# Kernel optimization log

Hardware: AMD Instinct MI355X
Metric: run time of the kernel (lower is better)

Reference implementation:

```python
import jax, jax.numpy as jnp
import numpy as np
import math

B, S, D, H = 2, 2048, 1024, 16
DK = D // H


def setup_inputs() -> dict:
    key = jax.random.key(0)
    k1, k2, k3, k4, k5, k6 = jax.random.split(key, 6)
    scale = 1.0 / math.sqrt(D)
    return {
        "query": jax.random.normal(k1, (B, S, D), dtype=jnp.float32),
        "key": jax.random.normal(k2, (B, S, D), dtype=jnp.float32),
        "value": jax.random.normal(k3, (B, S, D), dtype=jnp.float32),
        "Wqkv": jax.random.normal(k4, (D, D), dtype=jnp.float32) * scale,
        "Wout": jax.random.normal(k5, (D, D), dtype=jnp.float32) * scale,
        "mask": jax.random.randint(k6, (B, 1, S, S), 0, 2, dtype=jnp.int32),
    }


def reference(query, key, value, Wqkv, Wout, mask):
    # Single shared QKV projection (same weight applied to q, k, v), no bias.
    q = query @ Wqkv.T
    k = key @ Wqkv.T
    v = value @ Wqkv.T
    # Faithful to the original: reshape (B, S, D) -> (B, H, S, DK) directly
    # (torch .reshape(n_batches, h, -1, d_k), NOT view+transpose).
    q = q.reshape(B, H, S, DK)
    k = k.reshape(B, H, S, DK)
    v = v.reshape(B, H, S, DK)
    scores = jnp.einsum("bhqd,bhkd->bhqk", q, k) / math.sqrt(DK)
    scores = jnp.where(mask == 0, jnp.float32(-1e9), scores)
    p_attn = jax.nn.softmax(scores, axis=-1)  # dropout is identity in eval
    x = jnp.einsum("bhqk,bhkd->bhqd", p_attn, v)  # [B,H,S,DK]
    x = x.transpose(0, 2, 1, 3).reshape(B, S, H * DK)
    return x @ Wout.T
```

## Files before the change

kernel.cpp:

```cpp
#include <hip/hip_runtime.h>
#include <stdint.h>


typedef __bf16 bf16;
typedef __bf16 bf16x8 __attribute__((ext_vector_type(8)));
typedef __bf16 bf16x4 __attribute__((ext_vector_type(4)));
typedef float f32x4 __attribute__((ext_vector_type(4)));

#define MFMA16(a, b, c) __builtin_amdgcn_mfma_f32_16x16x32_bf16((a), (b), (c), 0, 0, 0)
#define EXP2(x) __builtin_amdgcn_exp2f(x)

static constexpr int BATCH = 2;
static constexpr int SEQ = 2048;
static constexpr int DIM = 1024;
static constexpr int DK = 64;
static constexpr float QSCALE = 0.125f * 1.44269504088896340736f;

__device__ inline void gload16(const void* g, void* l) {
  __builtin_amdgcn_global_load_lds((const __attribute__((address_space(1))) void*)g,
                                   (__attribute__((address_space(3))) void*)l, 16, 0, 0);
}

__global__ __launch_bounds__(256) void prep_kernel(
    const int* __restrict__ mask, unsigned long long* __restrict__ bits,
    const float* __restrict__ sq, const float* __restrict__ sk, const float* __restrict__ sv,
    const float* __restrict__ swq, const float* __restrict__ swo,
    bf16* __restrict__ dq, bf16* __restrict__ dk, bf16* __restrict__ dv,
    bf16* __restrict__ dwq, bf16* __restrict__ dwo) {
  const int bid = blockIdx.x;
  const int tid = threadIdx.x;
  if (bid < 8192) {
    const int lane = tid & 63, wv = tid >> 6;
    const int ebase = (bid * 4 + wv) * 256;
    unsigned long long w[4];
#pragma unroll
    for (int j = 0; j < 4; ++j) {
      int m = mask[ebase + j * 64 + lane];
      w[j] = __ballot(m != 0);
    }
    if (lane == 0) {
#pragma unroll
      for (int j = 0; j < 4; ++j) bits[(ebase >> 6) + j] = w[j];
    }
    return;
  }
  int r = bid - 8192;
  const float* s;
  bf16* d;
  int i;
  if (r < 6144) {
    s = (r < 2048) ? sq : (r < 4096) ? sk : sv;
    d = (r < 2048) ? dq : (r < 4096) ? dk : dv;
    i = (r & 2047) * 256 + tid;
  } else {
    r -= 6144;
    s = (r < 512) ? swq : swo;
    d = (r < 512) ? dwq : dwo;
    i = (r & 511) * 256 + tid;
  }
  const float4 a = ((const float4*)s)[2 * i];
  const float4 b = ((const float4*)s)[2 * i + 1];
  bf16x8 v;
  v[0] = (bf16)a.x;
  v[1] = (bf16)a.y;
  v[2] = (bf16)a.z;
  v[3] = (bf16)a.w;
  v[4] = (bf16)b.x;
  v[5] = (bf16)b.y;
  v[6] = (bf16)b.z;
  v[7] = (bf16)b.w;
  ((bf16x8*)d)[i] = v;
}

template <int BM, int BN, int NBX, int NBY, int NBZ, int MINW, typename TC>
__global__ __launch_bounds__(256, MINW) void gemm_bt_lds(
    const bf16* __restrict__ A0, const bf16* __restrict__ A1, const bf16* __restrict__ A2,
    const bf16* __restrict__ W, TC* __restrict__ C0, TC* __restrict__ C1, TC* __restrict__ C2,
    float scale0) {
  constexpr int K = 1024, N = 1024;
  constexpr int MT = BM / 32, NT = BN / 32;
  constexpr int PA = BM / 64, PB = BN / 64;
  constexpr int NB = NBX * NBY * NBZ;
  __shared__ __align__(16) bf16 As[2][BM * 32];
  __shared__ __align__(16) bf16 Bs[2][BN * 32];

  const int lin = blockIdx.x + NBX * (blockIdx.y + NBY * blockIdx.z);
  const int l = (lin & 7) * (NB / 8) + (lin >> 3);
  const int lx = l % NBX;
  const int ly = (l / NBX) % NBY;
  const int lz = l / (NBX * NBY);

  const bf16* A = (lz == 0) ? A0 : (lz == 1) ? A1 : A2;
  TC* C = (lz == 0) ? C0 : (lz == 1) ? C1 : C2;
  const float sc = (lz == 0) ? scale0 : 1.0f;

  const int tid = threadIdx.x;
  const int lane = tid & 63;
  const int wv = tid >> 6;
  const int wm = wv >> 1, wn = wv & 1;
  const int lrow = lane & 15, quad = lane >> 4;
  const int m0 = ly * BM, n0 = lx * BN;

  const int r0 = tid >> 2, c0 = (tid & 3) * 8;
  const bf16* pa[PA];
  const bf16* pb[PB];
#pragma unroll
  for (int p = 0; p < PA; ++p) pa[p] = A + (size_t)(m0 + p * 64 + r0) * K + c0;
#pragma unroll
  for (int p = 0; p < PB; ++p) pb[p] = W + (size_t)(n0 + p * 64 + r0) * K + c0;

  const f32x4 fz = {0.f, 0.f, 0.f, 0.f};
  f32x4 acc[MT][NT];
#pragma unroll
  for (int i = 0; i < MT; ++i)
#pragma unroll
    for (int j = 0; j < NT; ++j) acc[i][j] = fz;

#pragma unroll
  for (int p = 0; p < PA; ++p) gload16(pa[p], &As[0][p * 2048 + tid * 8]);
#pragma unroll
  for (int p = 0; p < PB; ++p) gload16(pb[p], &Bs[0][p * 2048 + tid * 8]);
  __syncthreads();

  for (int t = 0; t < K / 32; ++t) {
    const int cur = t & 1;
    if (t + 1 < K / 32) {
      const int k1 = (t + 1) * 32;
#pragma unroll
      for (int p = 0; p < PA; ++p) gload16(pa[p] + k1, &As[cur ^ 1][p * 2048 + tid * 8]);
#pragma unroll
      for (int p = 0; p < PB; ++p) gload16(pb[p] + k1, &Bs[cur ^ 1][p * 2048 + tid * 8]);
    }
    bf16x8 af[MT], bfr[NT];
#pragma unroll
    for (int mt = 0; mt < MT; ++mt)
      af[mt] = *(const bf16x8*)(&As[cur][(wm * (BM / 2) + mt * 16 + lrow) * 32 + quad * 8]);
#pragma unroll
    for (int nt = 0; nt < NT; ++nt)
      bfr[nt] = *(const bf16x8*)(&Bs[cur][(wn * (BN / 2) + nt * 16 + lrow) * 32 + quad * 8]);
#pragma unroll
    for (int mt = 0; mt < MT; ++mt)
#pragma unroll
      for (int nt = 0; nt < NT; ++nt) acc[mt][nt] = MFMA16(af[mt], bfr[nt], acc[mt][nt]);
    __syncthreads();
  }

#pragma unroll
  for (int mt = 0; mt < MT; ++mt) {
    const int gm = m0 + wm * (BM / 2) + mt * 16 + quad * 4;
#pragma unroll
    for (int nt = 0; nt < NT; ++nt) {
      const int gn = n0 + wn * (BN / 2) + nt * 16 + lrow;
#pragma unroll
      for (int r = 0; r < 4; ++r) C[(size_t)(gm + r) * N + gn] = (TC)(acc[mt][nt][r] * sc);
    }
  }
}

__global__ __launch_bounds__(256, 2) void attn_kernel(const bf16* __restrict__ Qg,
                                                      const bf16* __restrict__ Kg,
                                                      const bf16* __restrict__ Vg,
                                                      const unsigned* __restrict__ bits,
                                                      bf16* __restrict__ Y) {
  constexpr int LQ = 72;
  constexpr int LP = 68;
  __shared__ bf16 Qs[128 * LQ];
  __shared__ bf16 Ks[64 * LQ];
  __shared__ bf16 Vts[64 * LQ];
  __shared__ bf16 Ps[4][32 * LP];

  const int tid = threadIdx.x;
  const int lane = tid & 63;
  const int wv = tid >> 6;
  const int lrow = lane & 15, quad = lane >> 4;
  const int bh = blockIdx.y;
  const int b = bh >> 4, h = bh & 15;
  const int q0 = blockIdx.x * 128;

  const bf16* Qh = Qg + (size_t)bh * (SEQ * DK);
  const bf16* Kh = Kg + (size_t)bh * (SEQ * DK);
  const bf16* Vh = Vg + (size_t)bh * (SEQ * DK);

#pragma unroll
  for (int i = 0; i < 4; ++i) {
    int s = tid + i * 256;
    int row = s >> 3, c8 = (s & 7) * 8;
    *(uint4*)(&Qs[row * LQ + c8]) = *(const uint4*)(Qh + (size_t)(q0 + row) * DK + c8);
  }

  const int krow = tid >> 3;
  const int kc8 = (tid & 7) * 8;
  const bf16* pk0 = Kh + (size_t)krow * DK + kc8;
  const bf16* pk1 = Kh + (size_t)(krow + 32) * DK + kc8;
  const int vn2 = tid & 31;
  const int vk2b = tid >> 5;
  const bf16* pv0 = Vh + (size_t)(vk2b + 0) * 2 * DK + vn2 * 2;
  const bf16* pv1 = Vh + (size_t)(vk2b + 8) * 2 * DK + vn2 * 2;
  const bf16* pv2 = Vh + (size_t)(vk2b + 16) * 2 * DK + vn2 * 2;
  const bf16* pv3 = Vh + (size_t)(vk2b + 24) * 2 * DK + vn2 * 2;

  uint4 kr0, kr1;
  uint32_t va[4], vb[4];

  kr0 = *(const uint4*)(pk0);
  kr1 = *(const uint4*)(pk1);
  va[0] = *(const uint32_t*)(pv0);
  vb[0] = *(const uint32_t*)(pv0 + DK);
  va[1] = *(const uint32_t*)(pv1);
  vb[1] = *(const uint32_t*)(pv1 + DK);
  va[2] = *(const uint32_t*)(pv2);
  vb[2] = *(const uint32_t*)(pv2 + DK);
  va[3] = *(const uint32_t*)(pv3);
  vb[3] = *(const uint32_t*)(pv3 + DK);
  *(uint4*)(&Ks[krow * LQ + kc8]) = kr0;
  *(uint4*)(&Ks[(krow + 32) * LQ + kc8]) = kr1;
#pragma unroll
  for (int i = 0; i < 4; ++i) {
    uint32_t t0 = (va[i] & 0xffffu) | (vb[i] << 16);
    uint32_t t1 = (va[i] >> 16) | (vb[i] & 0xffff0000u);
    *(uint32_t*)(&Vts[(vn2 * 2) * LQ + (vk2b + i * 8) * 2]) = t0;
    *(uint32_t*)(&Vts[(vn2 * 2 + 1) * LQ + (vk2b + i * 8) * 2]) = t1;
  }
  __syncthreads();

  bf16x8 qf[2][2];
#pragma unroll
  for (int nt = 0; nt < 2; ++nt)
#pragma unroll
    for (int ks = 0; ks < 2; ++ks)
      qf[nt][ks] = *(const bf16x8*)(&Qs[(wv * 32 + nt * 16 + lrow) * LQ + ks * 32 + quad * 8]);
  __syncthreads();

  const f32x4 fz = {0.f, 0.f, 0.f, 0.f};
  f32x4 of_t[4][2];
#pragma unroll
  for (int i = 0; i < 4; ++i)
#pragma unroll
    for (int j = 0; j < 2; ++j) of_t[i][j] = fz;
  float lsum[2] = {0.f, 0.f};

  const unsigned* bitrow = bits + (size_t)b * SEQ * (SEQ / 32);

  for (int kt = 0; kt < 32; ++kt) {
    const int cur = kt & 1;
    bf16* kb = cur ? Qs : Ks;
    bf16* vbuf = cur ? (Qs + 64 * LQ) : Vts;
    if (kt + 1 < 32) {
      const size_t adv = (size_t)(kt + 1) * 64 * DK;
      kr0 = *(const uint4*)(pk0 + adv);
      kr1 = *(const uint4*)(pk1 + adv);
      va[0] = *(const uint32_t*)(pv0 + adv);
      vb[0] = *(const uint32_t*)(pv0 + adv + DK);
      va[1] = *(const uint32_t*)(pv1 + adv);
      vb[1] = *(const uint32_t*)(pv1 + adv + DK);
      va[2] = *(const uint32_t*)(pv2 + adv);
      vb[2] = *(const uint32_t*)(pv2 + adv + DK);
      va[3] = *(const uint32_t*)(pv3 + adv);
      vb[3] = *(const uint32_t*)(pv3 + adv + DK);
    }
    uint2 mwn[2];
#pragma unroll
    for (int nt = 0; nt < 2; ++nt) {
      int row = q0 + wv * 32 + nt * 16 + lrow;
      mwn[nt] = *(const uint2*)(bitrow + (size_t)row * (SEQ / 32) + kt * 2);
    }

    f32x4 st[4][2];
#pragma unroll
    for (int mt = 0; mt < 4; ++mt)
#pragma unroll
      for (int nt = 0; nt < 2; ++nt) st[mt][nt] = fz;
#pragma unroll
    for (int ks = 0; ks < 2; ++ks) {
#pragma unroll
      for (int mt = 0; mt < 4; ++mt) {
        bf16x8 kfv = *(const bf16x8*)(kb + (mt * 16 + lrow) * LQ + ks * 32 + quad * 8);
#pragma unroll
        for (int nt = 0; nt < 2; ++nt) st[mt][nt] = MFMA16(kfv, qf[nt][ks], st[mt][nt]);
      }
    }

#pragma unroll
    for (int nt = 0; nt < 2; ++nt) {
      uint32_t ux = mwn[nt].x >> (quad * 4);
      uint32_t uy = mwn[nt].y >> (quad * 4);
      float psum = 0.f;
#pragma unroll
      for (int mt = 0; mt < 4; ++mt) {
        uint32_t u = (mt & 2) ? uy : ux;
        int sh = (mt & 1) << 4;
        bf16x4 pk;
#pragma unroll
        for (int r = 0; r < 4; ++r) {
          float p = EXP2(st[mt][nt][r]);
          p = ((u >> (sh + r)) & 1u) ? p : 0.f;
          psum += p;
          pk[r] = (bf16)p;
        }
        *(bf16x4*)(&Ps[wv][(nt * 16 + lrow) * LP + mt * 16 + quad * 4]) = pk;
      }
      lsum[nt] += psum;
    }

#pragma unroll
    for (int ks = 0; ks < 2; ++ks) {
      bf16x8 avf[4], bpf[2];
#pragma unroll
      for (int dkt = 0; dkt < 4; ++dkt)
        avf[dkt] = *(const bf16x8*)(vbuf + (dkt * 16 + lrow) * LQ + ks * 32 + quad * 8);
#pragma unroll
      for (int rt = 0; rt < 2; ++rt)
        bpf[rt] = *(const bf16x8*)(&Ps[wv][(rt * 16 + lrow) * LP + ks * 32 + quad * 8]);
#pragma unroll
      for (int dkt = 0; dkt < 4; ++dkt)
#pragma unroll
        for (int rt = 0; rt < 2; ++rt) of_t[dkt][rt] = MFMA16(avf[dkt], bpf[rt], of_t[dkt][rt]);
    }

    if (kt + 1 < 32) {
      bf16* kbn = cur ? Ks : Qs;
      bf16* vbn = cur ? Vts : (Qs + 64 * LQ);
      *(uint4*)(kbn + krow * LQ + kc8) = kr0;
      *(uint4*)(kbn + (krow + 32) * LQ + kc8) = kr1;
#pragma unroll
      for (int i = 0; i < 4; ++i) {
        uint32_t t0 = (va[i] & 0xffffu) | (vb[i] << 16);
        uint32_t t1 = (va[i] >> 16) | (vb[i] & 0xffff0000u);
        *(uint32_t*)(vbn + (vn2 * 2) * LQ + (vk2b + i * 8) * 2) = t0;
        *(uint32_t*)(vbn + (vn2 * 2 + 1) * LQ + (vk2b + i * 8) * 2) = t1;
      }
    }
    __syncthreads();
  }

  float linv[2];
#pragma unroll
  for (int nt = 0; nt < 2; ++nt) {
    float v = lsum[nt];
    v += __shfl_xor(v, 16);
    v += __shfl_xor(v, 32);
    linv[nt] = 1.0f / fmaxf(v, 1e-20f);
  }

#pragma unroll
  for (int dkt = 0; dkt < 4; ++dkt)
#pragma unroll
    for (int rt = 0; rt < 2; ++rt) {
      bf16x4 o;
#pragma unroll
      for (int j = 0; j < 4; ++j) o[j] = (bf16)(of_t[dkt][rt][j] * linv[rt]);
      const int row = q0 + wv * 32 + rt * 16 + lrow;
      *(bf16x4*)(&Y[((size_t)b * SEQ + row) * DIM + h * 64 + dkt * 16 + quad * 4]) = o;
    }
}

extern "C" void kernel_launch(void* const* d_in, const int* in_sizes, int n_in,
                              void* d_out, int out_size, void* d_ws, size_t ws_size,
                              hipStream_t stream) {
  const float* query = (const float*)d_in[0];
  const float* key = (const float*)d_in[1];
  const float* value = (const float*)d_in[2];
  const float* Wqkv = (const float*)d_in[3];
  const float* Wout = (const float*)d_in[4];
  const int* mask = (const int*)d_in[5];
  float* out = (float*)d_out;

  char* ws = (char*)d_ws;
  bf16* qin = (bf16*)(ws);
  bf16* kin = (bf16*)(ws + 8388608);
  bf16* vin = (bf16*)(ws + 16777216);
  bf16* Wq = (bf16*)(ws + 25165824);
  bf16* Wo = (bf16*)(ws + 27262976);
  bf16* q = (bf16*)(ws + 29360128);
  bf16* k = (bf16*)(ws + 37748736);
  bf16* v = (bf16*)(ws + 46137344);
  bf16* y = (bf16*)(ws);
  unsigned long long* bits64 = (unsigned long long*)(ws + 54525952);

  prep_kernel<<<15360, 256, 0, stream>>>(mask, bits64, query, key, value, Wqkv, Wout,
                                         qin, kin, vin, Wq, Wo);

  gemm_bt_lds<64, 128, 8, 64, 3, 4, bf16>
      <<<dim3(8, 64, 3), 256, 0, stream>>>(qin, kin, vin, Wq, q, k, v, QSCALE);

  attn_kernel<<<dim3(16, 32), 256, 0, stream>>>(q, k, v, (const unsigned*)bits64, y);

  gemm_bt_lds<64, 128, 8, 64, 1, 2, float>
      <<<dim3(8, 64, 1), 256, 0, stream>>>(y, y, y, Wo, out, out, out, 1.0f);
}
```

Measured before the change: 249.2 us.

## Split attention over two key chunks with a separate combine kernel

Adds a split-K attention kernel that splits the key sequence into two halves along a third grid dimension, doubling the number of blocks. Each block writes fp32 partial outputs and row sums, and a new combine kernel adds the two halves, normalises and converts to bf16. The aim is better use of the GPU's compute units during attention, which previously launched only 512 blocks. In exchange it adds roughly 32 MB of fp32 partial-output writes plus their reads, and an extra kernel launch. The new path runs only when the workspace is large enough; otherwise the original kernel path is kept.

```diff
diff --git a/kernel.cpp b/kernel.cpp
--- a/kernel.cpp
+++ b/kernel.cpp
@@ -354,6 +354,230 @@
     }
 }
 
+__global__ __launch_bounds__(256, 4) void attn_split_kernel(
+    const bf16* __restrict__ Qg, const bf16* __restrict__ Kg, const bf16* __restrict__ Vg,
+    const unsigned* __restrict__ bits, float* __restrict__ Op, float* __restrict__ Lp) {
+  constexpr int LQ = 72;
+  constexpr int LP = 68;
+  __shared__ bf16 Ks[64 * LQ];
+  __shared__ bf16 Vts[64 * LQ];
+  __shared__ bf16 Ps[4][32 * LP];
+
+  const int tid = threadIdx.x;
+  const int lane = tid & 63;
+  const int wv = tid >> 6;
+  const int lrow = lane & 15, quad = lane >> 4;
+  const int bh = blockIdx.y;
+  const int b = bh >> 4, h = bh & 15;
+  const int q0 = blockIdx.x * 128;
+  const int z = blockIdx.z;
+  const int kt0 = z * 16;
+
+  const bf16* Qh = Qg + (size_t)bh * (SEQ * DK);
+  const bf16* Kh = Kg + (size_t)bh * (SEQ * DK);
+  const bf16* Vh = Vg + (size_t)bh * (SEQ * DK);
+
+  bf16x8 qf[2][2];
+#pragma unroll
+  for (int nt = 0; nt < 2; ++nt)
+#pragma unroll
+    for (int ks = 0; ks < 2; ++ks)
+      qf[nt][ks] =
+          *(const bf16x8*)(Qh + (size_t)(q0 + wv * 32 + nt * 16 + lrow) * DK + ks * 32 + quad * 8);
+
+  const int krow = tid >> 3;
+  const int kc8 = (tid & 7) * 8;
+  const bf16* pk0 = Kh + (size_t)krow * DK + kc8;
+  const bf16* pk1 = Kh + (size_t)(krow + 32) * DK + kc8;
+  const int vn2 = tid & 31;
+  const int vk2b = tid >> 5;
+  const bf16* pv0 = Vh + (size_t)(vk2b + 0) * 2 * DK + vn2 * 2;
+  const bf16* pv1 = Vh + (size_t)(vk2b + 8) * 2 * DK + vn2 * 2;
+  const bf16* pv2 = Vh + (size_t)(vk2b + 16) * 2 * DK + vn2 * 2;
+  const bf16* pv3 = Vh + (size_t)(vk2b + 24) * 2 * DK + vn2 * 2;
+
+  uint4 kr0, kr1;
+  uint32_t va[4], vb[4];
+
+  {
+    const size_t adv = (size_t)kt0 * 64 * DK;
+    kr0 = *(const uint4*)(pk0 + adv);
+    kr1 = *(const uint4*)(pk1 + adv);
+    va[0] = *(const uint32_t*)(pv0 + adv);
+    vb[0] = *(const uint32_t*)(pv0 + adv + DK);
+    va[1] = *(const uint32_t*)(pv1 + adv);
+    vb[1] = *(const uint32_t*)(pv1 + adv + DK);
+    va[2] = *(const uint32_t*)(pv2 + adv);
+    vb[2] = *(const uint32_t*)(pv2 + adv + DK);
+    va[3] = *(const uint32_t*)(pv3 + adv);
+    vb[3] = *(const uint32_t*)(pv3 + adv + DK);
+    *(uint4*)(&Ks[krow * LQ + kc8]) = kr0;
+    *(uint4*)(&Ks[(krow + 32) * LQ + kc8]) = kr1;
+#pragma unroll
+    for (int i = 0; i < 4; ++i) {
+      uint32_t t0 = (va[i] & 0xffffu) | (vb[i] << 16);
+      uint32_t t1 = (va[i] >> 16) | (vb[i] & 0xffff0000u);
+      *(uint32_t*)(&Vts[(vn2 * 2) * LQ + (vk2b + i * 8) * 2]) = t0;
+      *(uint32_t*)(&Vts[(vn2 * 2 + 1) * LQ + (vk2b + i * 8) * 2]) = t1;
+    }
+  }
+  __syncthreads();
+
+  const f32x4 fz = {0.f, 0.f, 0.f, 0.f};
+  f32x4 of_t[4][2];
+#pragma unroll
+  for (int i = 0; i < 4; ++i)
+#pragma unroll
+    for (int j = 0; j < 2; ++j) of_t[i][j] = fz;
+  float lsum[2] = {0.f, 0.f};
+
+  const unsigned* bitrow = bits + (size_t)b * SEQ * (SEQ / 32);
+
+  for (int it = 0; it < 16; ++it) {
+    const int kt = kt0 + it;
+    if (it + 1 < 16) {
+      const size_t adv = (size_t)(kt + 1) * 64 * DK;
+      kr0 = *(const uint4*)(pk0 + adv);
+      kr1 = *(const uint4*)(pk1 + adv);
+      va[0] = *(const uint32_t*)(pv0 + adv);
+      vb[0] = *(const uint32_t*)(pv0 + adv + DK);
+      va[1] = *(const uint32_t*)(pv1 + adv);
+      vb[1] = *(const uint32_t*)(pv1 + adv + DK);
+      va[2] = *(const uint32_t*)(pv2 + adv);
+      vb[2] = *(const uint32_t*)(pv2 + adv + DK);
+      va[3] = *(const uint32_t*)(pv3 + adv);
+      vb[3] = *(const uint32_t*)(pv3 + adv + DK);
+    }
+    uint2 mwn[2];
+#pragma unroll
+    for (int nt = 0; nt < 2; ++nt) {
+      int row = q0 + wv * 32 + nt * 16 + lrow;
+      mwn[nt] = *(const uint2*)(bitrow + (size_t)row * (SEQ / 32) + kt * 2);
+    }
+
+    f32x4 st[4][2];
+#pragma unroll
+    for (int mt = 0; mt < 4; ++mt)
+#pragma unroll
+      for (int nt = 0; nt < 2; ++nt) st[mt][nt] = fz;
+#pragma unroll
+    for (int ks = 0; ks < 2; ++ks) {
+#pragma unroll
+      for (int mt = 0; mt < 4; ++mt) {
+        bf16x8 kfv = *(const bf16x8*)(&Ks[(mt * 16 + lrow) * LQ + ks * 32 + quad * 8]);
+#pragma unroll
+        for (int nt = 0; nt < 2; ++nt) st[mt][nt] = MFMA16(kfv, qf[nt][ks], st[mt][nt]);
+      }
+    }
+
+#pragma unroll
+    for (int nt = 0; nt < 2; ++nt) {
+      uint32_t ux = mwn[nt].x >> (quad * 4);
+      uint32_t uy = mwn[nt].y >> (quad * 4);
+      float psum = 0.f;
+#pragma unroll
+      for (int mt = 0; mt < 4; ++mt) {
+        uint32_t u = (mt & 2) ? uy : ux;
+        int sh = (mt & 1) << 4;
+        bf16x4 pk;
+#pragma unroll
+        for (int r = 0; r < 4; ++r) {
+          float p = EXP2(st[mt][nt][r]);
+          p = ((u >> (sh + r)) & 1u) ? p : 0.f;
+          psum += p;
+          pk[r] = (bf16)p;
+        }
+        *(bf16x4*)(&Ps[wv][(nt * 16 + lrow) * LP + mt * 16 + quad * 4]) = pk;
+      }
+      lsum[nt] += psum;
+    }
+
+#pragma unroll
+    for (int ks = 0; ks < 2; ++ks) {
+      bf16x8 avf[4], bpf[2];
+#pragma unroll
+      for (int dkt = 0; dkt < 4; ++dkt)
+        avf[dkt] = *(const bf16x8*)(&Vts[(dkt * 16 + lrow) * LQ + ks * 32 + quad * 8]);
+#pragma unroll
+      for (int rt = 0; rt < 2; ++rt)
+        bpf[rt] = *(const bf16x8*)(&Ps[wv][(rt * 16 + lrow) * LP + ks * 32 + quad * 8]);
+#pragma unroll
+      for (int dkt = 0; dkt < 4; ++dkt)
+#pragma unroll
+        for (int rt = 0; rt < 2; ++rt) of_t[dkt][rt] = MFMA16(avf[dkt], bpf[rt], of_t[dkt][rt]);
+    }
+
+    __syncthreads();
+    if (it + 1 < 16) {
+      *(uint4*)(&Ks[krow * LQ + kc8]) = kr0;
+      *(uint4*)(&Ks[(krow + 32) * LQ + kc8]) = kr1;
+#pragma unroll
+      for (int i = 0; i < 4; ++i) {
+        uint32_t t0 = (va[i] & 0xffffu) | (vb[i] << 16);
+        uint32_t t1 = (va[i] >> 16) | (vb[i] & 0xffff0000u);
+        *(uint32_t*)(&Vts[(vn2 * 2) * LQ + (vk2b + i * 8) * 2]) = t0;
+        *(uint32_t*)(&Vts[(vn2 * 2 + 1) * LQ + (vk2b + i * 8) * 2]) = t1;
+      }
+    }
+    __syncthreads();
+  }
+
+  float lt[2];
+#pragma unroll
+  for (int nt = 0; nt < 2; ++nt) {
+    float v = lsum[nt];
+    v += __shfl_xor(v, 16);
+    v += __shfl_xor(v, 32);
+    lt[nt] = v;
+  }
+
+  float* OpZ = Op + (size_t)z * (BATCH * SEQ * DIM);
+#pragma unroll
+  for (int dkt = 0; dkt < 4; ++dkt)
+#pragma unroll
+    for (int rt = 0; rt < 2; ++rt) {
+      const int row = q0 + wv * 32 + rt * 16 + lrow;
+      *(f32x4*)(&OpZ[((size_t)b * SEQ + row) * DIM + h * 64 + dkt * 16 + quad * 4]) =
+          of_t[dkt][rt];
+    }
+  if (quad == 0) {
+#pragma unroll
+    for (int nt = 0; nt < 2; ++nt) {
+      const int row = q0 + wv * 32 + nt * 16 + lrow;
+      Lp[((size_t)z * 32 + bh) * SEQ + row] = lt[nt];
+    }
+  }
+}
+
+__global__ __launch_bounds__(256) void combine_kernel(const float* __restrict__ Op,
+                                                      const float* __restrict__ Lp,
+                                                      bf16* __restrict__ y) {
+  const int i8 = blockIdx.x * 256 + threadIdx.x;
+  const size_t i = (size_t)i8 * 8;
+  const int rowg = (int)(i / DIM);
+  const int h = ((int)(i % DIM)) >> 6;
+  const int b = rowg >> 11;
+  const int s = rowg & (SEQ - 1);
+  const float l = Lp[((size_t)(b * 16 + h)) * SEQ + s] +
+                  Lp[((size_t)(32 + b * 16 + h)) * SEQ + s];
+  const float inv = 1.0f / fmaxf(l, 1e-20f);
+  constexpr size_t HALF4 = (size_t)BATCH * SEQ * DIM / 4;
+  const float4 a0 = ((const float4*)Op)[i / 4];
+  const float4 a1 = ((const float4*)Op)[i / 4 + 1];
+  const float4 c0 = ((const float4*)Op)[HALF4 + i / 4];
+  const float4 c1 = ((const float4*)Op)[HALF4 + i / 4 + 1];
+  bf16x8 o;
+  o[0] = (bf16)((a0.x + c0.x) * inv);
+  o[1] = (bf16)((a0.y + c0.y) * inv);
+  o[2] = (bf16)((a0.z + c0.z) * inv);
+  o[3] = (bf16)((a0.w + c0.w) * inv);
+  o[4] = (bf16)((a1.x + c1.x) * inv);
+  o[5] = (bf16)((a1.y + c1.y) * inv);
+  o[6] = (bf16)((a1.z + c1.z) * inv);
+  o[7] = (bf16)((a1.w + c1.w) * inv);
+  ((bf16x8*)y)[i8] = o;
+}
+
 extern "C" void kernel_launch(void* const* d_in, const int* in_sizes, int n_in,
                               void* d_out, int out_size, void* d_ws, size_t ws_size,
                               hipStream_t stream) {
@@ -366,25 +590,49 @@
   float* out = (float*)d_out;
 
   char* ws = (char*)d_ws;
-  bf16* qin = (bf16*)(ws);
-  bf16* kin = (bf16*)(ws + 8388608);
-  bf16* vin = (bf16*)(ws + 16777216);
-  bf16* Wq = (bf16*)(ws + 25165824);
-  bf16* Wo = (bf16*)(ws + 27262976);
-  bf16* q = (bf16*)(ws + 29360128);
-  bf16* k = (bf16*)(ws + 37748736);
-  bf16* v = (bf16*)(ws + 46137344);
-  bf16* y = (bf16*)(ws);
-  unsigned long long* bits64 = (unsigned long long*)(ws + 54525952);
-
-  prep_kernel<<<15360, 256, 0, stream>>>(mask, bits64, query, key, value, Wqkv, Wout,
-                                         qin, kin, vin, Wq, Wo);
-
-  gemm_bt_lds<64, 128, 8, 64, 3, 4, bf16>
-      <<<dim3(8, 64, 3), 256, 0, stream>>>(qin, kin, vin, Wq, q, k, v, QSCALE);
-
-  attn_kernel<<<dim3(16, 32), 256, 0, stream>>>(q, k, v, (const unsigned*)bits64, y);
-
-  gemm_bt_lds<64, 128, 8, 64, 1, 2, float>
-      <<<dim3(8, 64, 1), 256, 0, stream>>>(y, y, y, Wo, out, out, out, 1.0f);
+  constexpr size_t WS_SPLIT = 62390272;
+
+  if (ws_size >= WS_SPLIT) {
+    float* Op = (float*)(ws);
+    bf16* qin = (bf16*)(ws);
+    bf16* kin = (bf16*)(ws + 8388608);
+    bf16* vin = (bf16*)(ws + 16777216);
+    bf16* Wq = (bf16*)(ws + 25165824);
+    bf16* q = (bf16*)(ws + 33554432);
+    bf16* k = (bf16*)(ws + 41943040);
+    bf16* v = (bf16*)(ws + 50331648);
+    unsigned long long* bits64 = (unsigned long long*)(ws + 58720256);
+    float* Lp = (float*)(ws + 59768832);
+    bf16* Wo = (bf16*)(ws + 60293120);
+    bf16* y = (bf16*)(ws + 33554432);
+
+    prep_kernel<<<15360, 256, 0, stream>>>(mask, bits64, query, key, value, Wqkv, Wout,
+                                           qin, kin, vin, Wq, Wo);
+    gemm_bt_lds<64, 128, 8, 64, 3, 4, bf16>
+        <<<dim3(8, 64, 3), 256, 0, stream>>>(qin, kin, vin, Wq, q, k, v, QSCALE);
+    attn_split_kernel<<<dim3(16, 32, 2), 256, 0, stream>>>(q, k, v, (const unsigned*)bits64,
+                                                           Op, Lp);
+    combine_kernel<<<2048, 256, 0, stream>>>(Op, Lp, y);
+    gemm_bt_lds<64, 128, 8, 64, 1, 2, float>
+        <<<dim3(8, 64, 1), 256, 0, stream>>>(y, y, y, Wo, out, out, out, 1.0f);
+  } else {
+    bf16* qin = (bf16*)(ws);
+    bf16* kin = (bf16*)(ws + 8388608);
+    bf16* vin = (bf16*)(ws + 16777216);
+    bf16* Wq = (bf16*)(ws + 25165824);
+    bf16* Wo = (bf16*)(ws + 27262976);
+    bf16* q = (bf16*)(ws + 29360128);
+    bf16* k = (bf16*)(ws + 37748736);
+    bf16* v = (bf16*)(ws + 46137344);
+    bf16* y = (bf16*)(ws);
+    unsigned long long* bits64 = (unsigned long long*)(ws + 54525952);
+
+    prep_kernel<<<15360, 256, 0, stream>>>(mask, bits64, query, key, value, Wqkv, Wout,
+                                           qin, kin, vin, Wq, Wo);
+    gemm_bt_lds<64, 128, 8, 64, 3, 4, bf16>
+        <<<dim3(8, 64, 3), 256, 0, stream>>>(qin, kin, vin, Wq, q, k, v, QSCALE);
+    attn_kernel<<<dim3(16, 32), 256, 0, stream>>>(q, k, v, (const unsigned*)bits64, y);
+    gemm_bt_lds<64, 128, 8, 64, 1, 2, float>
+        <<<dim3(8, 64, 1), 256, 0, stream>>>(y, y, y, Wo, out, out, out, 1.0f);
+  }
 }
```

Measured after the change: 248.9 us. About the same (-0.1%).
